# Optimization experiments

Measured on AMD Instinct MI355X. Metric: run time of the kernel, lower is better.

## Reference

```python
import jax, jax.numpy as jnp
import numpy as np

B, S, H, DH, W, G, M = 2, 4096, 12, 64, 256, 64, 256
D = H * DH  # 768
VOCAB = 50282
NEG = -1e9


def setup_inputs() -> dict:
    key = jax.random.key(0)
    ks = jax.random.split(key, 16)
    f = lambda k, shp, s=0.02: jax.random.normal(k, shp, jnp.float32) * s
    return {
        'input_ids': jax.random.randint(ks[0], (B, S), 0, VOCAB, jnp.int32),
        'attn_mask': jnp.ones((B, S), jnp.float32),
        'html_idx': jnp.sort(jax.random.randint(ks[1], (B, M), 0, S, jnp.int32), axis=-1),
        'embed': f(ks[2], (VOCAB, D), 1.0),
        'Wq': f(ks[3], (D, D)), 'bq': jnp.zeros((D,), jnp.float32),
        'Wk': f(ks[4], (D, D)), 'bk': jnp.zeros((D,), jnp.float32),
        'Wv': f(ks[5], (D, D)), 'bv': jnp.zeros((D,), jnp.float32),
        'Wo': f(ks[6], (D, D)), 'bo': jnp.zeros((D,), jnp.float32),
        'gamma': jnp.ones((D,), jnp.float32), 'beta': jnp.zeros((D,), jnp.float32),
        'Wp': f(ks[7], (D, D)), 'bp': jnp.zeros((D,), jnp.float32),
        'Wa': f(ks[8], (D, 3)), 'ba': jnp.zeros((3,), jnp.float32),
        'Ws': f(ks[9], (D, 2)), 'bs': jnp.zeros((2,), jnp.float32),
    }


def _band_shift(t, n_chunks):
    # t: [..., n_chunks+2, W, ...chunked along axis -3/-2]; gather 3 neighbor chunks
    return jnp.concatenate([t[..., i:i + n_chunks, :, :] for i in range(3)], axis=-2)


def longformer_hpt(input_ids, attn_mask, html_idx, embed, Wq, bq, Wk, bk, Wv, bv,
                   Wo, bo, gamma, beta, Wp, bp, Wa, ba, Ws, bs):
    x = embed[input_ids]  # [B,S,D]
    heads = lambda t: t.reshape(B, S, H, DH).transpose(0, 2, 1, 3)  # [B,H,S,DH]
    q, k, v = heads(x @ Wq + bq), heads(x @ Wk + bk), heads(x @ Wv + bv)
    scale = 1.0 / np.sqrt(DH).astype(np.float32)
    C = S // W  # chunks

    # --- sliding-window (banded) attention, one-sided window W ---
    kp = jnp.pad(k, ((0, 0), (0, 0), (W, W), (0, 0))).reshape(B, H, C + 2, W, DH)
    vp = jnp.pad(v, ((0, 0), (0, 0), (W, W), (0, 0))).reshape(B, H, C + 2, W, DH)
    k3 = _band_shift(kp, C)  # [B,H,C,3W,DH]
    v3 = _band_shift(vp, C)
    qc = q.reshape(B, H, C, W, DH)
    sb = jnp.einsum('bhcqd,bhckd->bhcqk', qc, k3) * scale  # [B,H,C,W,3W]

    ii = jnp.arange(W)[:, None]
    jj = jnp.arange(3 * W)[None, :]
    band_ok = jnp.abs(jj - W - ii) <= W  # [W,3W]
    keypos = jnp.arange(C)[:, None] * W - W + jnp.arange(3 * W)[None, :]  # [C,3W]
    kvalid = (keypos >= 0) & (keypos < S) & (keypos >= G)  # global keys handled separately
    mp = jnp.pad(attn_mask, ((0, 0), (W, W))).reshape(B, C + 2, W)
    m3 = jnp.concatenate([mp[:, i:i + C] for i in range(3)], axis=2)  # [B,C,3W]
    mask = band_ok[None, :, :] & kvalid[:, None, :] & (m3[:, :, None, :] > 0)[..., :, :].reshape(B, C, 1, 3 * W).astype(bool) if False else (band_ok[None, None, :, :] & kvalid[None, :, None, :] & (m3[:, :, None, :] > 0))  # [B,C,W,3W]
    sb = jnp.where(mask[:, None], sb, NEG).reshape(B, H, S, 3 * W)

    # --- all tokens also attend to the G global tokens ---
    kg, vg = k[:, :, :G], v[:, :, :G]
    sg = jnp.einsum('bhsd,bhgd->bhsg', q, kg) * scale
    sg = jnp.where(attn_mask[:, None, None, :G] > 0, sg, NEG)

    p = jax.nn.softmax(jnp.concatenate([sg, sb], -1), -1)  # [B,H,S,G+3W]
    pg, pb = p[..., :G], p[..., G:].reshape(B, H, C, W, 3 * W)
    out = (jnp.einsum('bhcqk,bhckd->bhcqd', pb, v3).reshape(B, H, S, DH)
           + jnp.einsum('bhsg,bhgd->bhsd', pg, vg))

    # --- global queries attend to everything ---
    sgl = jnp.einsum('bhgd,bhsd->bhgs', q[:, :, :G], k) * scale
    sgl = jnp.where(attn_mask[:, None, None, :] > 0, sgl, NEG)
    outg = jnp.einsum('bhgs,bhsd->bhgd', jax.nn.softmax(sgl, -1), v)
    out = jnp.concatenate([outg, out[:, :, G:]], axis=2)

    ctx = out.transpose(0, 2, 1, 3).reshape(B, S, D)
    h = x + ctx @ Wo + bo
    mu = h.mean(-1, keepdims=True)
    var = ((h - mu) ** 2).mean(-1, keepdims=True)
    hn = (h - mu) / jnp.sqrt(var + 1e-5) * gamma + beta  # last_hidden [B,S,D]

    # probes (ans_probe: Linear(768,3)+Sigmoid, span_probe: Linear(768,2)+Sigmoid)
    ans = jax.nn.sigmoid(hn @ Wa + ba)
    span = jax.nn.sigmoid(hn @ Ws + bs)

    # ReIndexer gather of HTML-element hidden states + ConditionCalculator
    hr = jnp.take_along_axis(hn, html_idx[:, :, None].astype(jnp.int32), axis=1)  # [B,M,D]
    t = jax.nn.relu(hr @ Wp + bp)
    cond = jax.nn.sigmoid(jnp.einsum('bqh,bch->bcq', hr, t))  # [B,M,M]
    return hn, ans, span, cond


def reference(input_ids, attn_mask, html_idx, embed, Wq, bq, Wk, bk, Wv, bv,
              Wo, bo, gamma, beta, Wp, bp, Wa, ba, Ws, bs):
    return longformer_hpt(input_ids, attn_mask, html_idx, embed, Wq, bq, Wk, bk,
                          Wv, bv, Wo, bo, gamma, beta, Wp, bp, Wa, ba, Ws, bs)
```

## Files before the change

kernel.cpp:

```cpp
#include <hip/hip_runtime.h>

typedef unsigned short u16;
typedef unsigned int   u32;
typedef __attribute__((ext_vector_type(8))) short s8v;
typedef __attribute__((ext_vector_type(8))) unsigned short us8;
typedef __attribute__((ext_vector_type(4))) unsigned short us4;
typedef __attribute__((ext_vector_type(4))) float f4v;

constexpr int BC  = 2;
constexpr int SL  = 4096;
constexpr int NH  = 12;
constexpr int HD  = 64;
constexpr int DM  = 768;
constexpr int WIN = 256;
constexpr int GLB = 64;
constexpr int QN  = 2304;
constexpr int KCH = 32;
constexpr float FOLD = 0.125f * 1.44269504088896f;
constexpr float NEGS = -1.0e9f;
constexpr float DEFER = 44.36f;

__device__ __forceinline__ float b2f(u16 b){ return __uint_as_float(((u32)b) << 16); }
__device__ __forceinline__ u16 f2b(float f){
  u32 u = __float_as_uint(f);
  return (u16)((u + 0x7fffu + ((u >> 16) & 1u)) >> 16);
}
__device__ __forceinline__ float wredsum(float v){
  #pragma unroll
  for (int o = 32; o > 0; o >>= 1) v += __shfl_xor(v, o, 64);
  return v;
}
__device__ __forceinline__ float sigf(float x){ return 1.f / (1.f + __expf(-x)); }

__global__ void pack_embed(const float* __restrict__ Wq, const float* __restrict__ Wk,
                           const float* __restrict__ Wv, const float* __restrict__ Wo,
                           const float* __restrict__ Wp,
                           const float* __restrict__ bq, const float* __restrict__ bk,
                           const float* __restrict__ bv,
                           u16* __restrict__ wt_qkv, u16* __restrict__ wt_o,
                           u16* __restrict__ wt_p, float* __restrict__ b_qkv,
                           const int* __restrict__ ids, const float* __restrict__ emb,
                           u16* __restrict__ xb)
{
  __shared__ float tile[64][65];
  const int bid = blockIdx.x;
  const int t = threadIdx.x;
  if (bid < 720){
    const int mi = bid / 144, rest = bid % 144;
    const int kt = rest / 12, ntc = rest % 12;
    const float* src = (mi==0)?Wq:(mi==1)?Wk:(mi==2)?Wv:(mi==3)?Wo:Wp;
    u16* dst = (mi<3) ? (wt_qkv + (size_t)mi*768*768) : ((mi==3) ? wt_o : wt_p);
    const int k0 = kt*64, n0 = ntc*64;
    #pragma unroll
    for (int i=0;i<4;i++){
      const int r = (t>>4) + i*16;
      float4 v = ((const float4*)(src + (long)(k0+r)*768 + n0))[t&15];
      tile[r][(t&15)*4+0] = v.x; tile[r][(t&15)*4+1] = v.y;
      tile[r][(t&15)*4+2] = v.z; tile[r][(t&15)*4+3] = v.w;
    }
    __syncthreads();
    const int n = t & 63, kc = (t>>6)*16;
    u32* d32 = (u32*)(dst + (long)(n0+n)*768 + k0 + kc);
    #pragma unroll
    for (int i=0;i<8;i++){
      d32[i] = (u32)f2b(tile[kc+2*i][n]) | ((u32)f2b(tile[kc+2*i+1][n]) << 16);
    }
    if (bid < 9){
      const int i = bid*256 + t;
      if (i < 2304) b_qkv[i] = (i < 768) ? bq[i] : (i < 1536) ? bk[i-768] : bv[i-1536];
    }
  } else {
    int e4 = (bid-720)*256 + t;
    int row = e4 / 192, d4 = e4 - row*192;
    int id = ids[row];
    float4 v = ((const float4*)(emb + (long)id*768))[d4];
    u32 p0 = (u32)f2b(v.x) | ((u32)f2b(v.y) << 16);
    u32 p1 = (u32)f2b(v.z) | ((u32)f2b(v.w) << 16);
    ((u32*)(xb + (long)row*768))[d4*2]   = p0;
    ((u32*)(xb + (long)row*768))[d4*2+1] = p1;
  }
}

__global__ void gather_hr(const int* __restrict__ hidx, const float* __restrict__ hn,
                          u16* __restrict__ hrb){
  int e = blockIdx.x*256 + threadIdx.x;
  if (e >= 512*768) return;
  int r = e / 768, d = e - r*768;
  int b = r >> 8;
  int idx = hidx[r];
  hrb[e] = f2b(hn[((long)(b*SL + idx))*768 + d]);
}

template<int MODE, bool SWZ>
__global__ __launch_bounds__(256, 2)
void gemm_bt(const u16* __restrict__ A, const u16* __restrict__ Bt,
             const float* __restrict__ bias, const u16* __restrict__ resB,
             float* __restrict__ outF, u16* __restrict__ outB,
             int M, int N, int K, long sA, long sB, long sO)
{
  const int bz = blockIdx.z;
  A  += (long)bz * sA;
  Bt += (long)bz * sB;
  int vid = blockIdx.x + gridDim.x*blockIdx.y;
  if constexpr (SWZ){
    const int chunk = (gridDim.x*gridDim.y) >> 3;
    vid = (vid & 7)*chunk + (vid >> 3);
  }
  const int n0 = (vid % gridDim.x) * 128;
  const int m0 = (vid / gridDim.x) * 128;
  __shared__ u16 lsA[128*64];
  __shared__ u16 lsB[128*64];
  const int t = threadIdx.x;
  const int w = t >> 6, lane = t & 63;
  const int wr = w >> 1, wc = w & 1;
  const int fr = lane & 15, fq = lane >> 4;

  f4v acc[4][4];
  #pragma unroll
  for (int i=0;i<4;i++)
    #pragma unroll
    for (int j=0;j<4;j++) acc[i][j] = (f4v)0.f;

  for (int k0 = 0; k0 < K; k0 += 64){
    #pragma unroll
    for (int i=0;i<4;i++){
      int e = (w*4+i)*512 + lane*8;
      int row = e >> 6, col = e & 63;
      __builtin_amdgcn_global_load_lds(
        (const __attribute__((address_space(1))) void*)(A + (long)(m0+row)*K + (k0+col)),
        (__attribute__((address_space(3))) void*)(&lsA[(w*4+i)*512]), 16, 0, 0);
      __builtin_amdgcn_global_load_lds(
        (const __attribute__((address_space(1))) void*)(Bt + (long)(n0+row)*K + (k0+col)),
        (__attribute__((address_space(3))) void*)(&lsB[(w*4+i)*512]), 16, 0, 0);
    }
    __syncthreads();
    #pragma unroll
    for (int kk = 0; kk < 2; kk++){
      s8v af[4], bfv[4];
      #pragma unroll
      for (int mi=0;mi<4;mi++)
        af[mi] = *(const s8v*)&lsA[(wr*64 + mi*16 + fr)*64 + kk*32 + fq*8];
      #pragma unroll
      for (int ni=0;ni<4;ni++)
        bfv[ni] = *(const s8v*)&lsB[(wc*64 + ni*16 + fr)*64 + kk*32 + fq*8];
      #pragma unroll
      for (int mi=0;mi<4;mi++)
        #pragma unroll
        for (int ni=0;ni<4;ni++)
          acc[mi][ni] = __builtin_amdgcn_mfma_f32_16x16x32_bf16(af[mi], bfv[ni], acc[mi][ni], 0, 0, 0);
    }
    __syncthreads();
  }
  #pragma unroll
  for (int mi=0;mi<4;mi++){
    #pragma unroll
    for (int ni=0;ni<4;ni++){
      #pragma unroll
      for (int r=0;r<4;r++){
        int row = m0 + wr*64 + mi*16 + fq*4 + r;
        int col = n0 + wc*64 + ni*16 + fr;
        float v = acc[mi][ni][r];
        if constexpr (MODE == 0){
          v += bias[col];
          outB[(long)row*N + col] = f2b(v);
        } else if constexpr (MODE == 1){
          v += bias[col] + b2f(resB[(long)row*N + col]);
          outB[(long)row*N + col] = f2b(v);
        } else if constexpr (MODE == 2){
          v = fmaxf(v + bias[col], 0.f);
          outB[(long)row*N + col] = f2b(v);
        } else {
          (outF + bz*sO)[(long)row*N + col] = sigf(v);
        }
      }
    }
  }
}

__global__ __launch_bounds__(256, 4)
void attn_band_mfma(const u16* __restrict__ qkv, const float* __restrict__ mask, u16* __restrict__ ctx)
{
  const int q0 = (blockIdx.x + 1) * 64;
  const int h = blockIdx.y, b = blockIdx.z;
  const int t = threadIdx.x;
  const int w = t >> 6, lane = t & 63;
  const int fq = lane >> 4, fr = lane & 15;

  __shared__ u16 lsK[64*64];
  __shared__ u16 lsVT[2][64*72];
  __shared__ u16 lsP[4][16*72];
  __shared__ float lsM[2][64];

  const long bq = (long)b*SL*QN;
  const u16* qrow = qkv + (bq + (long)(q0 + w*16 + fr)*QN) + h*HD;
  s8v aq[2];
  aq[0] = *(const s8v*)(qrow + fq*8);
  aq[1] = *(const s8v*)(qrow + 32 + fq*8);

  s8v ones_bf;
  {
    const short o = (fr == 0) ? (short)0x3F80 : (short)0;
    #pragma unroll
    for (int j=0;j<8;j++) ones_bf[j] = o;
  }

  const u16* kq = qkv + bq + DM + h*HD;
  const u16* vq = qkv + bq + 2*DM + h*HD;
  const float* mrow = mask + b*SL;

  const int ti_lo = (q0 < 320) ? ((320 - q0) >> 6) : 0;
  const int ti_hi_raw = (4352 - q0) >> 6;
  const int ti_hi = ti_hi_raw < 9 ? ti_hi_raw : 9;
  const int NTT = 1 + (ti_hi - ti_lo);
  const int kb0 = q0 - 256 + ti_lo*64;

  f4v out[4];
  f4v outl = (f4v)0.f;
  #pragma unroll
  for (int n=0;n<4;n++) out[n] = (f4v)0.f;
  float m = -3.0e38f;

  const int k2 = lane & 31, dq = lane >> 5;
  const int dd0 = w*8 + dq*4;

  us4 va0, vb0, va1, vb1;
  auto stage_issue = [&](int i, int vbuf){
    const int k0 = (i == 0) ? 0 : kb0 + (i-1)*64;
    if (t < 64) lsM[vbuf][t] = mrow[k0 + t];
    #pragma unroll
    for (int j=0;j<2;j++){
      const int r = (w*2+j)*8 + (lane>>3);
      const int d = ((lane&7) ^ (lane>>3))*8;
      __builtin_amdgcn_global_load_lds(
        (const __attribute__((address_space(1))) void*)(kq + (long)(k0+r)*QN + d),
        (__attribute__((address_space(3))) void*)(&lsK[(w*2+j)*512]), 16, 0, 0);
    }
    const u16* v0 = vq + (long)(k0+2*k2)*QN;
    const u16* v1 = vq + (long)(k0+2*k2+1)*QN;
    va0 = *(const us4*)(v0 + dd0);
    vb0 = *(const us4*)(v1 + dd0);
    va1 = *(const us4*)(v0 + dd0 + 32);
    vb1 = *(const us4*)(v1 + dd0 + 32);
  };

  stage_issue(0, 0);
  int cur = 0;
  for (int i = 0; i < NTT; i++){
    const int k0 = (i == 0) ? 0 : kb0 + (i-1)*64;
    #pragma unroll
    for (int j=0;j<4;j++){
      const u32 pk0 = (u32)va0[j] | ((u32)vb0[j] << 16);
      *(u32*)&lsVT[cur][(dd0+j)*72 + 2*k2] = pk0;
      const u32 pk1 = (u32)va1[j] | ((u32)vb1[j] << 16);
      *(u32*)&lsVT[cur][(dd0+32+j)*72 + 2*k2] = pk1;
    }
    __syncthreads();

    f4v s[4];
    #pragma unroll
    for (int n=0;n<4;n++) s[n] = (f4v)0.f;
    #pragma unroll
    for (int kk=0;kk<2;kk++){
      #pragma unroll
      for (int n=0;n<4;n++){
        s8v bf = *(const s8v*)&lsK[(16*n+fr)*64 + (((kk*4+fq) ^ (fr&7))<<3)];
        s[n] = __builtin_amdgcn_mfma_f32_16x16x32_bf16(aq[kk], bf, s[n], 0,0,0);
      }
    }
    __syncthreads();
    if (i+1 < NTT) stage_issue(i+1, cur^1);

    const bool isg = (i == 0);
    const int dlt = k0 - q0 - w*16;
    const bool maskAll = __all(lsM[cur][lane] > 0.f);
    const bool fullOK = maskAll && (isg || (dlt >= -241 && dlt <= 193));
    if (!fullOK){
      #pragma unroll
      for (int n=0;n<4;n++){
        const int kcol = 16*n + fr;
        const float mk = lsM[cur][kcol];
        #pragma unroll
        for (int r=0;r<4;r++){
          const int dd = k0 + kcol - (q0 + w*16 + fq*4 + r);
          const bool valid = (mk > 0.f) && (isg || (dd >= -WIN && dd <= WIN));
          s[n][r] = valid ? s[n][r] : NEGS;
        }
      }
    }
    float rmloc = fmaxf(fmaxf(fmaxf(s[0][0],s[0][1]),fmaxf(s[0][2],s[0][3])),
                        fmaxf(fmaxf(s[1][0],s[1][1]),fmaxf(s[1][2],s[1][3])));
    rmloc = fmaxf(rmloc, fmaxf(fmaxf(fmaxf(s[2][0],s[2][1]),fmaxf(s[2][2],s[2][3])),
                               fmaxf(fmaxf(s[3][0],s[3][1]),fmaxf(s[3][2],s[3][3]))));
    if (__any(rmloc > m + DEFER)){
      float rm = rmloc;
      rm = fmaxf(rm, __shfl_xor(rm, 1, 64));
      rm = fmaxf(rm, __shfl_xor(rm, 2, 64));
      rm = fmaxf(rm, __shfl_xor(rm, 4, 64));
      rm = fmaxf(rm, __shfl_xor(rm, 8, 64));
      const float mn = fmaxf(m, rm);
      const float sf = exp2f((m - mn)*FOLD);
      m = mn;
      outl *= sf;
      #pragma unroll
      for (int n=0;n<4;n++)
        #pragma unroll
        for (int r=0;r<4;r++) out[n][r] *= sf;
    }
    const float mF = m * FOLD;
    u16* lsPw = lsP[w];
    #pragma unroll
    for (int r=0;r<4;r++){
      const float p0 = exp2f(fmaf(s[0][r], FOLD, -mF));
      const float p1 = exp2f(fmaf(s[1][r], FOLD, -mF));
      const float p2 = exp2f(fmaf(s[2][r], FOLD, -mF));
      const float p3 = exp2f(fmaf(s[3][r], FOLD, -mF));
      u32 a, c;
      asm("v_cvt_pk_bf16_f32 %0, %1, %2" : "=v"(a) : "v"(p0), "v"(p1));
      asm("v_cvt_pk_bf16_f32 %0, %1, %2" : "=v"(c) : "v"(p2), "v"(p3));
      const int row = (fq*4+r)*72;
      lsPw[row + fr]      = (u16)a;
      lsPw[row + 16 + fr] = (u16)(a >> 16);
      lsPw[row + 32 + fr] = (u16)c;
      lsPw[row + 48 + fr] = (u16)(c >> 16);
    }
    s8v ap[2];
    ap[0] = *(const s8v*)&lsPw[fr*72 + fq*8];
    ap[1] = *(const s8v*)&lsPw[fr*72 + 32 + fq*8];
    #pragma unroll
    for (int kk=0;kk<2;kk++){
      #pragma unroll
      for (int n=0;n<4;n++){
        s8v bv = *(const s8v*)&lsVT[cur][(16*n+fr)*72 + kk*32 + fq*8];
        out[n] = __builtin_amdgcn_mfma_f32_16x16x32_bf16(ap[kk], bv, out[n], 0,0,0);
      }
      outl = __builtin_amdgcn_mfma_f32_16x16x32_bf16(ap[kk], ones_bf, outl, 0,0,0);
    }
    cur ^= 1;
  }
  float linv[4];
  #pragma unroll
  for (int r=0;r<4;r++) linv[r] = 1.f / __shfl(outl[r], lane & 48, 64);
  u16* cb = ctx + (((long)(b*SL) + q0 + w*16 + fq*4))*DM + h*HD + fr;
  #pragma unroll
  for (int n=0;n<4;n++)
    #pragma unroll
    for (int r=0;r<4;r++)
      cb[(long)r*DM + 16*n] = f2b(out[n][r]*linv[r]);
}

__global__ __launch_bounds__(256, 4)
void attn_global_part(const u16* __restrict__ qkv, const float* __restrict__ mask,
                      float* __restrict__ pout, float* __restrict__ pml)
{
  const int ck = blockIdx.x;
  const int h = blockIdx.y, b = blockIdx.z;
  const int bh = b*NH + h;
  const int t = threadIdx.x;
  const int w = t >> 6, lane = t & 63;
  const int fq = lane >> 4, fr = lane & 15;

  __shared__ u16 lsK[64*64];
  __shared__ u16 lsVT[2][64*72];
  __shared__ u16 lsP[4][16*72];
  __shared__ float lsM[2][64];

  const long bq = (long)b*SL*QN;
  const u16* qrow = qkv + (bq + (long)(w*16 + fr)*QN) + h*HD;
  s8v aq[2];
  aq[0] = *(const s8v*)(qrow + fq*8);
  aq[1] = *(const s8v*)(qrow + 32 + fq*8);

  s8v ones_bf;
  {
    const short o = (fr == 0) ? (short)0x3F80 : (short)0;
    #pragma unroll
    for (int j=0;j<8;j++) ones_bf[j] = o;
  }

  const u16* kq = qkv + bq + DM + h*HD;
  const u16* vq = qkv + bq + 2*DM + h*HD;
  const float* mrow = mask + b*SL;

  f4v out[4];
  f4v outl = (f4v)0.f;
  #pragma unroll
  for (int n=0;n<4;n++) out[n] = (f4v)0.f;
  float m = -3.0e38f;

  const int k2 = lane & 31, dq = lane >> 5;
  const int dd0 = w*8 + dq*4;

  us4 va0, vb0, va1, vb1;
  auto stage_issue = [&](int i, int vbuf){
    const int k0 = ck*128 + i*64;
    if (t < 64) lsM[vbuf][t] = mrow[k0 + t];
    #pragma unroll
    for (int j=0;j<2;j++){
      const int r = (w*2+j)*8 + (lane>>3);
      const int d = ((lane&7) ^ (lane>>3))*8;
      __builtin_amdgcn_global_load_lds(
        (const __attribute__((address_space(1))) void*)(kq + (long)(k0+r)*QN + d),
        (__attribute__((address_space(3))) void*)(&lsK[(w*2+j)*512]), 16, 0, 0);
    }
    const u16* v0 = vq + (long)(k0+2*k2)*QN;
    const u16* v1 = vq + (long)(k0+2*k2+1)*QN;
    va0 = *(const us4*)(v0 + dd0);
    vb0 = *(const us4*)(v1 + dd0);
    va1 = *(const us4*)(v0 + dd0 + 32);
    vb1 = *(const us4*)(v1 + dd0 + 32);
  };

  stage_issue(0, 0);
  int cur = 0;
  for (int i = 0; i < 2; i++){
    #pragma unroll
    for (int j=0;j<4;j++){
      const u32 pk0 = (u32)va0[j] | ((u32)vb0[j] << 16);
      *(u32*)&lsVT[cur][(dd0+j)*72 + 2*k2] = pk0;
      const u32 pk1 = (u32)va1[j] | ((u32)vb1[j] << 16);
      *(u32*)&lsVT[cur][(dd0+32+j)*72 + 2*k2] = pk1;
    }
    __syncthreads();

    f4v s[4];
    #pragma unroll
    for (int n=0;n<4;n++) s[n] = (f4v)0.f;
    #pragma unroll
    for (int kk=0;kk<2;kk++){
      #pragma unroll
      for (int n=0;n<4;n++){
        s8v bf = *(const s8v*)&lsK[(16*n+fr)*64 + (((kk*4+fq) ^ (fr&7))<<3)];
        s[n] = __builtin_amdgcn_mfma_f32_16x16x32_bf16(aq[kk], bf, s[n], 0,0,0);
      }
    }
    __syncthreads();
    if (i+1 < 2) stage_issue(i+1, cur^1);

    const bool fullOK = __all(lsM[cur][lane] > 0.f);
    if (!fullOK){
      #pragma unroll
      for (int n=0;n<4;n++){
        const float mk = lsM[cur][16*n + fr];
        #pragma unroll
        for (int r=0;r<4;r++)
          s[n][r] = (mk > 0.f) ? s[n][r] : NEGS;
      }
    }
    float rmloc = fmaxf(fmaxf(fmaxf(s[0][0],s[0][1]),fmaxf(s[0][2],s[0][3])),
                        fmaxf(fmaxf(s[1][0],s[1][1]),fmaxf(s[1][2],s[1][3])));
    rmloc = fmaxf(rmloc, fmaxf(fmaxf(fmaxf(s[2][0],s[2][1]),fmaxf(s[2][2],s[2][3])),
                               fmaxf(fmaxf(s[3][0],s[3][1]),fmaxf(s[3][2],s[3][3]))));
    if (__any(rmloc > m + DEFER)){
      float rm = rmloc;
      rm = fmaxf(rm, __shfl_xor(rm, 1, 64));
      rm = fmaxf(rm, __shfl_xor(rm, 2, 64));
      rm = fmaxf(rm, __shfl_xor(rm, 4, 64));
      rm = fmaxf(rm, __shfl_xor(rm, 8, 64));
      const float mn = fmaxf(m, rm);
      const float sf = exp2f((m - mn)*FOLD);
      m = mn;
      outl *= sf;
      #pragma unroll
      for (int n=0;n<4;n++)
        #pragma unroll
        for (int r=0;r<4;r++) out[n][r] *= sf;
    }
    const float mF = m * FOLD;
    u16* lsPw = lsP[w];
    #pragma unroll
    for (int r=0;r<4;r++){
      const float p0 = exp2f(fmaf(s[0][r], FOLD, -mF));
      const float p1 = exp2f(fmaf(s[1][r], FOLD, -mF));
      const float p2 = exp2f(fmaf(s[2][r], FOLD, -mF));
      const float p3 = exp2f(fmaf(s[3][r], FOLD, -mF));
      u32 a, c;
      asm("v_cvt_pk_bf16_f32 %0, %1, %2" : "=v"(a) : "v"(p0), "v"(p1));
      asm("v_cvt_pk_bf16_f32 %0, %1, %2" : "=v"(c) : "v"(p2), "v"(p3));
      const int row = (fq*4+r)*72;
      lsPw[row + fr]      = (u16)a;
      lsPw[row + 16 + fr] = (u16)(a >> 16);
      lsPw[row + 32 + fr] = (u16)c;
      lsPw[row + 48 + fr] = (u16)(c >> 16);
    }
    s8v ap[2];
    ap[0] = *(const s8v*)&lsPw[fr*72 + fq*8];
    ap[1] = *(const s8v*)&lsPw[fr*72 + 32 + fq*8];
    #pragma unroll
    for (int kk=0;kk<2;kk++){
      #pragma unroll
      for (int n=0;n<4;n++){
        s8v bv = *(const s8v*)&lsVT[cur][(16*n+fr)*72 + kk*32 + fq*8];
        out[n] = __builtin_amdgcn_mfma_f32_16x16x32_bf16(ap[kk], bv, out[n], 0,0,0);
      }
      outl = __builtin_amdgcn_mfma_f32_16x16x32_bf16(ap[kk], ones_bf, outl, 0,0,0);
    }
    cur ^= 1;
  }
  float* pob = pout + ((long)(ck*BC*NH + bh))*64*64;
  #pragma unroll
  for (int n=0;n<4;n++)
    #pragma unroll
    for (int r=0;r<4;r++)
      pob[(w*16 + fq*4 + r)*64 + 16*n + fr] = out[n][r];
  if (fr == 0){
    float* pmb = pml + ((long)(ck*BC*NH + bh))*128;
    #pragma unroll
    for (int r=0;r<4;r++){
      pmb[(w*16 + fq*4 + r)*2 + 0] = m * FOLD;
      pmb[(w*16 + fq*4 + r)*2 + 1] = outl[r];
    }
  }
}

__global__ __launch_bounds__(256, 2)
void attn_global_combine(const float* __restrict__ pout, const float* __restrict__ pml,
                         u16* __restrict__ ctx)
{
  const int bh = blockIdx.x;
  const int b = bh / NH, h = bh % NH;
  const int t = threadIdx.x;
  __shared__ float wgt[KCH][64];
  __shared__ float rl[64];
  if (t < 64){
    float mc[KCH], lc[KCH];
    #pragma unroll
    for (int c = 0; c < KCH; c++){
      const float* pmb = pml + ((long)(c*BC*NH + bh))*128 + t*2;
      mc[c] = pmb[0]; lc[c] = pmb[1];
    }
    float M = mc[0];
    #pragma unroll
    for (int c = 1; c < KCH; c++) M = fmaxf(M, mc[c]);
    float L = 0.f;
    #pragma unroll
    for (int c = 0; c < KCH; c++){
      const float wv = exp2f(mc[c] - M);
      wgt[c][t] = wv;
      L += lc[c]*wv;
    }
    rl[t] = 1.f/L;
  }
  __syncthreads();
  const int row = t >> 2, dseg = t & 3;
  float acc[16];
  #pragma unroll
  for (int i=0;i<16;i++) acc[i] = 0.f;
  for (int c = 0; c < KCH; c++){
    const float wv = wgt[c][row];
    const float4* pb = (const float4*)(pout + ((long)(c*BC*NH + bh)*64 + row)*64 + dseg*16);
    #pragma unroll
    for (int i = 0; i < 4; i++){
      float4 v = pb[i];
      acc[i*4+0] += v.x*wv; acc[i*4+1] += v.y*wv;
      acc[i*4+2] += v.z*wv; acc[i*4+3] += v.w*wv;
    }
  }
  u16* cr = ctx + ((long)(b*SL + row))*DM + h*HD + dseg*16;
  const float r = rl[row];
  #pragma unroll
  for (int i = 0; i < 16; i += 2){
    u32 pk = (u32)f2b(acc[i]*r) | ((u32)f2b(acc[i+1]*r) << 16);
    *(u32*)(cr + i) = pk;
  }
}

__global__ __launch_bounds__(384, 2)
void ln_heads(const u16* __restrict__ hb, const float* __restrict__ gamma, const float* __restrict__ beta,
              const float* __restrict__ Wa, const float* __restrict__ ba,
              const float* __restrict__ Wsp, const float* __restrict__ bsp,
              float* __restrict__ hn, float* __restrict__ ans, float* __restrict__ span)
{
  const int r = blockIdx.x;
  const int t = threadIdx.x, lane = t & 63, w = t >> 6;
  __shared__ float red[12];
  __shared__ float dred[6][5];
  const u32 pk = ((const u32*)(hb + (long)r*DM))[t];
  const float v0 = b2f((u16)(pk & 0xffff));
  const float v1 = b2f((u16)(pk >> 16));
  float sum = wredsum(v0 + v1);
  float sq  = wredsum(v0*v0 + v1*v1);
  if (lane == 0){ red[w] = sum; red[6+w] = sq; }
  __syncthreads();
  float mu = 0.f, msq = 0.f;
  #pragma unroll
  for (int i=0;i<6;i++){ mu += red[i]; msq += red[6+i]; }
  mu *= (1.f/768.f); msq *= (1.f/768.f);
  const float rstd = rsqrtf(msq - mu*mu + 1e-5f);
  const int i0 = 2*t, i1 = 2*t+1;
  const float y0 = (v0 - mu)*rstd*gamma[i0] + beta[i0];
  const float y1 = (v1 - mu)*rstd*gamma[i1] + beta[i1];
  ((float2*)(hn + (long)r*DM))[t] = make_float2(y0, y1);
  float pa0 = y0*Wa[i0*3+0] + y1*Wa[i1*3+0];
  float pa1 = y0*Wa[i0*3+1] + y1*Wa[i1*3+1];
  float pa2 = y0*Wa[i0*3+2] + y1*Wa[i1*3+2];
  float ps0 = y0*Wsp[i0*2+0] + y1*Wsp[i1*2+0];
  float ps1 = y0*Wsp[i0*2+1] + y1*Wsp[i1*2+1];
  pa0 = wredsum(pa0); pa1 = wredsum(pa1); pa2 = wredsum(pa2);
  ps0 = wredsum(ps0); ps1 = wredsum(ps1);
  if (lane == 0){ dred[w][0]=pa0; dred[w][1]=pa1; dred[w][2]=pa2; dred[w][3]=ps0; dred[w][4]=ps1; }
  __syncthreads();
  if (t == 0){
    float A0=0,A1=0,A2=0,S0=0,S1=0;
    #pragma unroll
    for (int i=0;i<6;i++){ A0+=dred[i][0]; A1+=dred[i][1]; A2+=dred[i][2]; S0+=dred[i][3]; S1+=dred[i][4]; }
    ans[(long)r*3+0]  = sigf(A0 + ba[0]);
    ans[(long)r*3+1]  = sigf(A1 + ba[1]);
    ans[(long)r*3+2]  = sigf(A2 + ba[2]);
    span[(long)r*2+0] = sigf(S0 + bsp[0]);
    span[(long)r*2+1] = sigf(S1 + bsp[1]);
  }
}

extern "C" void kernel_launch(void* const* d_in, const int* in_sizes, int n_in,
                              void* d_out, int out_size, void* d_ws, size_t ws_size,
                              hipStream_t stream)
{
  const int*   input_ids = (const int*)  d_in[0];
  const float* attn_mask = (const float*)d_in[1];
  const int*   html_idx  = (const int*)  d_in[2];
  const float* embed     = (const float*)d_in[3];
  const float* Wq = (const float*)d_in[4];  const float* bq = (const float*)d_in[5];
  const float* Wk = (const float*)d_in[6];  const float* bk = (const float*)d_in[7];
  const float* Wv = (const float*)d_in[8];  const float* bv = (const float*)d_in[9];
  const float* Wo = (const float*)d_in[10]; const float* bo = (const float*)d_in[11];
  const float* gamma = (const float*)d_in[12]; const float* beta = (const float*)d_in[13];
  const float* Wp = (const float*)d_in[14]; const float* bp = (const float*)d_in[15];
  const float* Wa = (const float*)d_in[16]; const float* ba = (const float*)d_in[17];
  const float* Wsp = (const float*)d_in[18]; const float* bsp = (const float*)d_in[19];

  char* ws = (char*)d_ws;
  size_t off = 0;
  auto take = [&](size_t bytes)->char*{
    char* p = ws + off; off += (bytes + 255) & ~(size_t)255; return p;
  };
  u16*   x_b    = (u16*)  take((size_t)8192*768*2);
  u16*   wt_qkv = (u16*)  take((size_t)2304*768*2);
  u16*   wt_o   = (u16*)  take((size_t)768*768*2);
  u16*   wt_p   = (u16*)  take((size_t)768*768*2);
  float* b_qkv  = (float*)take(2304*4);
  u16*   qkv_b  = (u16*)  take((size_t)8192*2304*2);
  u16*   ctx_b  = (u16*)  take((size_t)8192*768*2);
  u16*   h_b    = (u16*)  take((size_t)8192*768*2);
  u16*   hr_b   = (u16*)  take((size_t)512*768*2);
  u16*   t_b    = (u16*)  take((size_t)512*768*2);
  float* pout   = (float*)take((size_t)KCH*BC*NH*64*64*4);
  float* pml    = (float*)take((size_t)KCH*BC*NH*128*4);

  float* out_hn   = (float*)d_out;
  float* out_ans  = out_hn  + (size_t)8192*768;
  float* out_span = out_ans + (size_t)8192*3;
  float* out_cond = out_span + (size_t)8192*2;

  pack_embed<<<6864, 256, 0, stream>>>(Wq, Wk, Wv, Wo, Wp, bq, bk, bv,
                                       wt_qkv, wt_o, wt_p, b_qkv,
                                       input_ids, embed, x_b);

  gemm_bt<0,true><<<dim3(18,64,1), 256, 0, stream>>>(x_b, wt_qkv, b_qkv, nullptr,
                                                nullptr, qkv_b, 8192, 2304, 768, 0,0,0);
  attn_band_mfma<<<dim3(63,12,2), 256, 0, stream>>>(qkv_b, attn_mask, ctx_b);
  attn_global_part<<<dim3(KCH,12,2), 256, 0, stream>>>(qkv_b, attn_mask, pout, pml);
  attn_global_combine<<<BC*NH, 256, 0, stream>>>(pout, pml, ctx_b);
  gemm_bt<1,true><<<dim3(6,64,1), 256, 0, stream>>>(ctx_b, wt_o, bo, x_b,
                                               nullptr, h_b, 8192, 768, 768, 0,0,0);
  ln_heads<<<8192, 384, 0, stream>>>(h_b, gamma, beta, Wa, ba, Wsp, bsp,
                                     out_hn, out_ans, out_span);
  gather_hr<<<1536, 256, 0, stream>>>(html_idx, out_hn, hr_b);
  gemm_bt<2,false><<<dim3(6,4,1), 256, 0, stream>>>(hr_b, wt_p, bp, nullptr,
                                              nullptr, t_b, 512, 768, 768, 0,0,0);
  gemm_bt<3,false><<<dim3(2,2,2), 256, 0, stream>>>(t_b, hr_b, nullptr, nullptr,
                                              out_cond, nullptr, 256, 256, 768,
                                              (long)256*768, (long)256*768, (long)256*256);
}
```

Baseline: 226.3 us.

## Keep softmax probabilities in registers by transposing QK MFMA and permuting V layout

The QK^T MFMA operands are swapped so each lane holds scores in the layout the PV MFMA's A operand needs. This removes the per-wave LDS round trip for the P matrix. The V transpose stores use a permuted column index so the key order matches the register-resident P fragment. The attention mask is now read per lane and turned into a wave ballot bitmask instead of going through shared memory. Row-max reductions need two extra shuffles because of the new layout, and correctness depends on the permutation exactly matching the MFMA fragment mapping.

```diff
diff --git a/kernel.cpp b/kernel.cpp
--- a/kernel.cpp
+++ b/kernel.cpp
@@ -2,6 +2,7 @@
 
 typedef unsigned short u16;
 typedef unsigned int   u32;
+typedef unsigned long long u64;
 typedef __attribute__((ext_vector_type(8))) short s8v;
 typedef __attribute__((ext_vector_type(8))) unsigned short us8;
 typedef __attribute__((ext_vector_type(4))) unsigned short us4;
@@ -188,8 +189,6 @@
 
   __shared__ u16 lsK[64*64];
   __shared__ u16 lsVT[2][64*72];
-  __shared__ u16 lsP[4][16*72];
-  __shared__ float lsM[2][64];
 
   const long bq = (long)b*SL*QN;
   const u16* qrow = qkv + (bq + (long)(q0 + w*16 + fr)*QN) + h*HD;
@@ -222,11 +221,14 @@
 
   const int k2 = lane & 31, dq = lane >> 5;
   const int dd0 = w*8 + dq*4;
+  const int kv = 2*k2;
+  const int cperm = (((kv>>4)>>1)<<5) + (((kv>>2)&3)<<3) + (((kv>>4)&1)<<2) + (kv&3);
 
   us4 va0, vb0, va1, vb1;
-  auto stage_issue = [&](int i, int vbuf){
+  float mval;
+  auto stage_issue = [&](int i){
     const int k0 = (i == 0) ? 0 : kb0 + (i-1)*64;
-    if (t < 64) lsM[vbuf][t] = mrow[k0 + t];
+    mval = mrow[k0 + lane];
     #pragma unroll
     for (int j=0;j<2;j++){
       const int r = (w*2+j)*8 + (lane>>3);
@@ -235,24 +237,24 @@
         (const __attribute__((address_space(1))) void*)(kq + (long)(k0+r)*QN + d),
         (__attribute__((address_space(3))) void*)(&lsK[(w*2+j)*512]), 16, 0, 0);
     }
-    const u16* v0 = vq + (long)(k0+2*k2)*QN;
-    const u16* v1 = vq + (long)(k0+2*k2+1)*QN;
+    const u16* v0 = vq + (long)(k0+kv)*QN;
+    const u16* v1 = vq + (long)(k0+kv+1)*QN;
     va0 = *(const us4*)(v0 + dd0);
     vb0 = *(const us4*)(v1 + dd0);
     va1 = *(const us4*)(v0 + dd0 + 32);
     vb1 = *(const us4*)(v1 + dd0 + 32);
   };
 
-  stage_issue(0, 0);
+  stage_issue(0);
   int cur = 0;
   for (int i = 0; i < NTT; i++){
     const int k0 = (i == 0) ? 0 : kb0 + (i-1)*64;
     #pragma unroll
     for (int j=0;j<4;j++){
       const u32 pk0 = (u32)va0[j] | ((u32)vb0[j] << 16);
-      *(u32*)&lsVT[cur][(dd0+j)*72 + 2*k2] = pk0;
+      *(u32*)&lsVT[cur][(dd0+j)*72 + cperm] = pk0;
       const u32 pk1 = (u32)va1[j] | ((u32)vb1[j] << 16);
-      *(u32*)&lsVT[cur][(dd0+32+j)*72 + 2*k2] = pk1;
+      *(u32*)&lsVT[cur][(dd0+32+j)*72 + cperm] = pk1;
     }
     __syncthreads();
 
@@ -264,25 +266,25 @@
       #pragma unroll
       for (int n=0;n<4;n++){
         s8v bf = *(const s8v*)&lsK[(16*n+fr)*64 + (((kk*4+fq) ^ (fr&7))<<3)];
-        s[n] = __builtin_amdgcn_mfma_f32_16x16x32_bf16(aq[kk], bf, s[n], 0,0,0);
+        s[n] = __builtin_amdgcn_mfma_f32_16x16x32_bf16(bf, aq[kk], s[n], 0,0,0);
       }
     }
     __syncthreads();
-    if (i+1 < NTT) stage_issue(i+1, cur^1);
+    const u64 mkb = __ballot(mval > 0.f);
+    if (i+1 < NTT) stage_issue(i+1);
 
     const bool isg = (i == 0);
     const int dlt = k0 - q0 - w*16;
-    const bool maskAll = __all(lsM[cur][lane] > 0.f);
-    const bool fullOK = maskAll && (isg || (dlt >= -241 && dlt <= 193));
+    const bool fullOK = (~mkb == 0ull) && (isg || (dlt >= -241 && dlt <= 193));
     if (!fullOK){
+      const int base = k0 + 4*fq - (q0 + w*16 + fr);
       #pragma unroll
       for (int n=0;n<4;n++){
-        const int kcol = 16*n + fr;
-        const float mk = lsM[cur][kcol];
         #pragma unroll
         for (int r=0;r<4;r++){
-          const int dd = k0 + kcol - (q0 + w*16 + fq*4 + r);
-          const bool valid = (mk > 0.f) && (isg || (dd >= -WIN && dd <= WIN));
+          const bool mb = (mkb >> (16*n + 4*fq + r)) & 1ull;
+          const int dd = base + 16*n + r;
+          const bool valid = mb && (isg || (dd >= -WIN && dd <= WIN));
           s[n][r] = valid ? s[n][r] : NEGS;
         }
       }
@@ -297,6 +299,8 @@
       rm = fmaxf(rm, __shfl_xor(rm, 2, 64));
       rm = fmaxf(rm, __shfl_xor(rm, 4, 64));
       rm = fmaxf(rm, __shfl_xor(rm, 8, 64));
+      rm = fmaxf(rm, __shfl_xor(rm, 16, 64));
+      rm = fmaxf(rm, __shfl_xor(rm, 32, 64));
       const float mn = fmaxf(m, rm);
       const float sf = exp2f((m - mn)*FOLD);
       m = mn;
@@ -307,34 +311,35 @@
         for (int r=0;r<4;r++) out[n][r] *= sf;
     }
     const float mF = m * FOLD;
-    u16* lsPw = lsP[w];
-    #pragma unroll
-    for (int r=0;r<4;r++){
-      const float p0 = exp2f(fmaf(s[0][r], FOLD, -mF));
-      const float p1 = exp2f(fmaf(s[1][r], FOLD, -mF));
-      const float p2 = exp2f(fmaf(s[2][r], FOLD, -mF));
-      const float p3 = exp2f(fmaf(s[3][r], FOLD, -mF));
-      u32 a, c;
-      asm("v_cvt_pk_bf16_f32 %0, %1, %2" : "=v"(a) : "v"(p0), "v"(p1));
-      asm("v_cvt_pk_bf16_f32 %0, %1, %2" : "=v"(c) : "v"(p2), "v"(p3));
-      const int row = (fq*4+r)*72;
-      lsPw[row + fr]      = (u16)a;
-      lsPw[row + 16 + fr] = (u16)(a >> 16);
-      lsPw[row + 32 + fr] = (u16)c;
-      lsPw[row + 48 + fr] = (u16)(c >> 16);
-    }
-    s8v ap[2];
-    ap[0] = *(const s8v*)&lsPw[fr*72 + fq*8];
-    ap[1] = *(const s8v*)&lsPw[fr*72 + 32 + fq*8];
-    #pragma unroll
-    for (int kk=0;kk<2;kk++){
-      #pragma unroll
-      for (int n=0;n<4;n++){
-        s8v bv = *(const s8v*)&lsVT[cur][(16*n+fr)*72 + kk*32 + fq*8];
-        out[n] = __builtin_amdgcn_mfma_f32_16x16x32_bf16(ap[kk], bv, out[n], 0,0,0);
-      }
-      outl = __builtin_amdgcn_mfma_f32_16x16x32_bf16(ap[kk], ones_bf, outl, 0,0,0);
-    }
+    float p00 = exp2f(fmaf(s[0][0], FOLD, -mF)), p01 = exp2f(fmaf(s[0][1], FOLD, -mF));
+    float p02 = exp2f(fmaf(s[0][2], FOLD, -mF)), p03 = exp2f(fmaf(s[0][3], FOLD, -mF));
+    float p10 = exp2f(fmaf(s[1][0], FOLD, -mF)), p11 = exp2f(fmaf(s[1][1], FOLD, -mF));
+    float p12 = exp2f(fmaf(s[1][2], FOLD, -mF)), p13 = exp2f(fmaf(s[1][3], FOLD, -mF));
+    float p20 = exp2f(fmaf(s[2][0], FOLD, -mF)), p21 = exp2f(fmaf(s[2][1], FOLD, -mF));
+    float p22 = exp2f(fmaf(s[2][2], FOLD, -mF)), p23 = exp2f(fmaf(s[2][3], FOLD, -mF));
+    float p30 = exp2f(fmaf(s[3][0], FOLD, -mF)), p31 = exp2f(fmaf(s[3][1], FOLD, -mF));
+    float p32 = exp2f(fmaf(s[3][2], FOLD, -mF)), p33 = exp2f(fmaf(s[3][3], FOLD, -mF));
+    u32 c0,c1,c2,c3,c4,c5,c6,c7;
+    asm("v_cvt_pk_bf16_f32 %0, %1, %2" : "=v"(c0) : "v"(p00), "v"(p01));
+    asm("v_cvt_pk_bf16_f32 %0, %1, %2" : "=v"(c1) : "v"(p02), "v"(p03));
+    asm("v_cvt_pk_bf16_f32 %0, %1, %2" : "=v"(c2) : "v"(p10), "v"(p11));
+    asm("v_cvt_pk_bf16_f32 %0, %1, %2" : "=v"(c3) : "v"(p12), "v"(p13));
+    asm("v_cvt_pk_bf16_f32 %0, %1, %2" : "=v"(c4) : "v"(p20), "v"(p21));
+    asm("v_cvt_pk_bf16_f32 %0, %1, %2" : "=v"(c5) : "v"(p22), "v"(p23));
+    asm("v_cvt_pk_bf16_f32 %0, %1, %2" : "=v"(c6) : "v"(p30), "v"(p31));
+    asm("v_cvt_pk_bf16_f32 %0, %1, %2" : "=v"(c7) : "v"(p32), "v"(p33));
+    s8v ap0, ap1;
+    { u32* u = (u32*)&ap0; u[0]=c0; u[1]=c1; u[2]=c2; u[3]=c3; }
+    { u32* u = (u32*)&ap1; u[0]=c4; u[1]=c5; u[2]=c6; u[3]=c7; }
+    #pragma unroll
+    for (int n=0;n<4;n++){
+      s8v bv0 = *(const s8v*)&lsVT[cur][(16*n+fr)*72 + fq*8];
+      out[n] = __builtin_amdgcn_mfma_f32_16x16x32_bf16(ap0, bv0, out[n], 0,0,0);
+      s8v bv1 = *(const s8v*)&lsVT[cur][(16*n+fr)*72 + 32 + fq*8];
+      out[n] = __builtin_amdgcn_mfma_f32_16x16x32_bf16(ap1, bv1, out[n], 0,0,0);
+    }
+    outl = __builtin_amdgcn_mfma_f32_16x16x32_bf16(ap0, ones_bf, outl, 0,0,0);
+    outl = __builtin_amdgcn_mfma_f32_16x16x32_bf16(ap1, ones_bf, outl, 0,0,0);
     cur ^= 1;
   }
   float linv[4];
```

New measurement: 223.3 us. No clear change (-1.3%).
